# Kernel tuning notes

Measured on AMD Instinct MI355X. Metric: run time of the kernel, lower is better.

The kernel has to match this reference:

```python
import jax, jax.numpy as jnp
import numpy as np

N_HEADS = 8
TANH_CLIP = 10.0
NEG = -1e9  # finite stand-in for -inf so log_softmax/vjp stay NaN-free


def setup_inputs() -> dict:
    key = jax.random.key(0)
    ks = jax.random.split(key, 8)
    B, N, D = 256, 1000, 128
    embeddings = jax.random.normal(ks[0], (B, N, D), dtype=jnp.float32)
    W_node = jax.random.normal(ks[1], (D, 3 * D), dtype=jnp.float32) * (1.0 / np.sqrt(D))
    W_fixed = jax.random.normal(ks[2], (D, D), dtype=jnp.float32) * (1.0 / np.sqrt(D))
    W_step = jax.random.normal(ks[3], (2 * D, D), dtype=jnp.float32) * (1.0 / np.sqrt(2 * D))
    W_out = jax.random.normal(ks[4], (D, D), dtype=jnp.float32) * (1.0 / np.sqrt(D))
    first_idx = jax.random.randint(ks[5], (B,), 0, N)
    last_idx = jax.random.randint(ks[6], (B,), 0, N)
    mask = jax.random.randint(ks[7], (B, N), 0, 2).astype(jnp.bool_)
    mask = mask.at[:, 0].set(False)  # guarantee at least one feasible node
    return {"embeddings": embeddings, "W_node": W_node, "W_fixed": W_fixed,
            "W_step": W_step, "W_out": W_out, "first_idx": first_idx,
            "last_idx": last_idx, "mask": mask}


def reference(embeddings, W_node, W_fixed, W_step, W_out, first_idx, last_idx, mask):
    # One pointer-network decode step (TSP variant of AttentionModel._get_log_p),
    # including the _precompute projections.
    B, N, D = embeddings.shape
    H = N_HEADS
    dk = D // H

    # _precompute: fixed context + glimpse K/V + logit key
    graph_embed = embeddings.mean(axis=1)                       # [B, D]
    fixed_ctx = graph_embed @ W_fixed                           # [B, D]
    kvl = embeddings @ W_node                                   # [B, N, 3D]
    K, V, logit_K = jnp.split(kvl, 3, axis=-1)                  # each [B, N, D]

    # step context: cat(first-node emb, last-node emb) -> project to D
    b = jnp.arange(B)
    step_ctx = jnp.concatenate([embeddings[b, first_idx], embeddings[b, last_idx]], axis=-1)  # [B, 2D]
    q = fixed_ctx + step_ctx @ W_step                           # [B, D]

    # masked multi-head glimpse attention (q_len = 1)
    qh = q.reshape(B, H, dk)                                    # [B, H, dk]
    Kh = K.reshape(B, N, H, dk)
    Vh = V.reshape(B, N, H, dk)
    compat = jnp.einsum('bhd,bnhd->bhn', qh, Kh) / np.sqrt(dk)  # [B, H, N]
    compat = jnp.where(mask[:, None, :], NEG, compat)           # mask_inner
    attn = jax.nn.softmax(compat, axis=-1)
    heads = jnp.einsum('bhn,bnhd->bhd', attn, Vh)               # [B, H, dk]
    glimpse = heads.reshape(B, D) @ W_out                       # [B, D]

    # single-head logit attention with tanh clipping
    logits = jnp.einsum('bd,bnd->bn', glimpse, logit_K) / np.sqrt(D)  # [B, N]
    logits = jnp.tanh(logits) * TANH_CLIP
    logits = jnp.where(mask, NEG, logits)                       # mask_logits
    return jax.nn.log_softmax(logits, axis=-1)                  # [B, N]
```

## Files before the change

### kernel.cpp

```cpp
#include <hip/hip_runtime.h>


#define NEG (-1e9f)

__global__ __launch_bounds__(512, 4) void k1_mean(
    const float* __restrict__ E, float* __restrict__ muP)
{
    const int bid = blockIdx.x;
    const int b = bid & 255, half = bid >> 8;
    const int blk = b * 2 + half;
    const int t = threadIdx.x;
    const int r0g = half * 500;
    __shared__ float4 sc[512];
    const float4* E4 = (const float4*)(E + (size_t)b * 128000);
    const int cm = t & 31, sm = t >> 5;
    float4 acc = make_float4(0.f, 0.f, 0.f, 0.f);
    for (int r = sm; r < 500; r += 16) {
        const float4 v = E4[(r0g + r) * 32 + cm];
        acc.x += v.x; acc.y += v.y; acc.z += v.z; acc.w += v.w;
    }
    sc[t] = acc;
    __syncthreads();
    if (t < 32) {
        float4 a = sc[t];
        #pragma unroll
        for (int s = 1; s < 16; ++s) {
            const float4 v = sc[s * 32 + t];
            a.x += v.x; a.y += v.y; a.z += v.z; a.w += v.w;
        }
        ((float4*)(muP + (size_t)blk * 128))[t] = a;
    }
}

__global__ __launch_bounds__(512, 2) void k2_attn(
    const float* __restrict__ E, const float* __restrict__ Wn,
    const float* __restrict__ Wf, const float* __restrict__ Ws,
    const int* __restrict__ fi, const int* __restrict__ li,
    const int* __restrict__ maskI, const unsigned char* __restrict__ maskB,
    const float* __restrict__ muP, float* __restrict__ Uw,
    float* __restrict__ lw)
{
    const int bid = blockIdx.x;
    const int b = bid & 255, half = bid >> 8;
    const int blk = b * 2 + half;
    const int i0 = b * 2, i1 = i0 + 1;
    const int t = threadIdx.x;
    const int r0g = half * 500;

    __shared__ float4 Et4[2048];
    __shared__ float4 qk4[256];
    __shared__ float4 pt4[128];
    __shared__ float4 mu4[32], e14[32], e24[32];
    __shared__ float q[128];
    __shared__ float qred[4][128];
    __shared__ float ct[64 * 9];
    __shared__ float redh[72];
    __shared__ int flagS;

    float* const mu  = (float*)mu4;
    float* const e1  = (float*)e14;
    float* const e2  = (float*)e24;
    float* const pt  = (float*)pt4;
    float* const qkf = (float*)qk4;
    float* const Etf = (float*)Et4;

    const float4* E4 = (const float4*)(E + (size_t)b * 128000);

    if (t == 0) flagS = 0;
    const uint4 dv = ((const uint4*)maskI)[t];
    const unsigned det = (dv.x | dv.y | dv.z | dv.w) & 0xFFFFFF00u;

    if (t < 128) {
        mu[t] = (muP[(size_t)i0 * 128 + t] + muP[(size_t)i1 * 128 + t])
                * (1.0f / 1000.0f);
    } else if (t < 160) {
        e14[t - 128] = E4[fi[b] * 32 + (t - 128)];
    } else if (t < 192) {
        e24[t - 160] = E4[li[b] * 32 + (t - 160)];
    }
    __syncthreads();
    if (det) atomicOr(&flagS, 1);

    {
        const int part = t >> 7, d = t & 127;
        float acc = 0.f;
        const int k0 = part * 96;
        for (int k = k0; k < k0 + 96; ++k) {
            const float s = (k < 128) ? mu[k] : (k < 256 ? e1[k - 128] : e2[k - 256]);
            const float w = (k < 128) ? Wf[k * 128 + d] : Ws[(k - 128) * 128 + d];
            acc += s * w;
        }
        qred[part][d] = acc;
    }
    __syncthreads();
    if (t < 128) q[t] = qred[0][t] + qred[1][t] + qred[2][t] + qred[3][t];
    __syncthreads();
    {
        const int j = t & 127, cg = t >> 7;
        const float qj = q[j];
        for (int c0 = 0; c0 < 128; c0 += 4) {
            const int c = c0 + cg;
            float v = Wn[c * 384 + j] * qj;
            v += __shfl_down(v, 8, 16);
            v += __shfl_down(v, 4, 16);
            v += __shfl_down(v, 2, 16);
            v += __shfl_down(v, 1, 16);
            if ((j & 15) == 0) {
                const int h = j >> 4, s = c >> 2;
                qkf[h * 128 + (s ^ (s >> 2)) * 4 + (c & 3)] = v * 0.25f;
            }
        }
    }
    __syncthreads();
    const bool useB = (flagS != 0);

    float eacc[8];
    #pragma unroll
    for (int h = 0; h < 8; ++h) eacc[h] = 0.f;
    float lacc = 0.f;
    const int rr = t >> 3, qq = t & 7;
    const int esl = t >> 7, ec = t & 127;

    for (int tile = 0; tile < 8; ++tile) {
        const int lr = tile * 64 + rr;
        const bool valid = (lr < 500);
        {
            float4 v[4];
            if (valid) {
                #pragma unroll
                for (int i = 0; i < 4; ++i) v[i] = E4[(r0g + lr) * 32 + qq * 4 + i];
            } else {
                #pragma unroll
                for (int i = 0; i < 4; ++i) v[i] = make_float4(0.f, 0.f, 0.f, 0.f);
            }
            float pch[8];
            #pragma unroll
            for (int h = 0; h < 8; ++h) pch[h] = 0.f;
            #pragma unroll
            for (int i = 0; i < 4; ++i) {
                const int grp = qq * 4 + i;
                Et4[rr * 32 + grp] = v[i];
                const int sg = grp ^ (grp >> 2);
                #pragma unroll
                for (int h = 0; h < 8; ++h) {
                    const float4 w = qk4[h * 32 + sg];
                    pch[h] += v[i].x * w.x + v[i].y * w.y + v[i].z * w.z + v[i].w * w.w;
                }
            }
            #pragma unroll
            for (int m = 1; m <= 4; m <<= 1) {
                #pragma unroll
                for (int h = 0; h < 8; ++h) pch[h] += __shfl_xor(pch[h], m, 8);
            }
            bool msk = !valid;
            if (valid) msk = useB ? (maskB[b * 1000 + r0g + lr] != 0)
                                  : (maskI[b * 1000 + r0g + lr] != 0);
            ct[rr * 9 + qq] = msk ? NEG : pch[qq];
        }
        __syncthreads();
        pt[(t >> 3) * 8 + (t & 7)] = __expf(ct[(t >> 3) * 9 + (t & 7)]);
        __syncthreads();
        {
            #pragma unroll
            for (int j = 0; j < 16; ++j) {
                const int r = esl * 16 + j;
                const float ev = Etf[r * 128 + ec];
                const float4 p0 = pt4[r * 2];
                const float4 p1 = pt4[r * 2 + 1];
                eacc[0] += p0.x * ev; eacc[1] += p0.y * ev;
                eacc[2] += p0.z * ev; eacc[3] += p0.w * ev;
                eacc[4] += p1.x * ev; eacc[5] += p1.y * ev;
                eacc[6] += p1.z * ev; eacc[7] += p1.w * ev;
            }
            if (t < 64) {
                const int h = t & 7, part = t >> 3;
                #pragma unroll
                for (int r = 0; r < 8; ++r) lacc += pt[(part * 8 + r) * 8 + h];
            }
        }
        __syncthreads();
    }

    #pragma unroll
    for (int h = 0; h < 8; ++h) Etf[esl * 1024 + h * 128 + ec] = eacc[h];
    if (t < 64) redh[(t >> 3) * 9 + (t & 7)] = lacc;
    __syncthreads();
    #pragma unroll
    for (int e = 0; e < 2; ++e) {
        const int idx = t + e * 512;
        Uw[(size_t)blk * 1024 + idx] =
            Etf[idx] + Etf[1024 + idx] + Etf[2048 + idx] + Etf[3072 + idx];
    }
    if (t < 8) {
        float s = 0.f;
        #pragma unroll
        for (int p = 0; p < 8; ++p) s += redh[p * 9 + t];
        lw[blk * 8 + t] = s;
    }
}

__global__ __launch_bounds__(1024) void k3_glimpse(
    const float* __restrict__ Wn, const float* __restrict__ Wo,
    const float* __restrict__ Uw, const float* __restrict__ lw,
    float* __restrict__ gpw)
{
    const int b = blockIdx.x;
    const int t = threadIdx.x;
    const int i0 = b * 2, i1 = i0 + 1;
    __shared__ float EbarF[1024];
    __shared__ float linv[8];
    __shared__ float heads[128], gl[128];
    __shared__ float qred[8][128];
    if (t < 8) linv[t] = 1.0f / (lw[i0 * 8 + t] + lw[i1 * 8 + t]);
    __syncthreads();
    EbarF[t] = (Uw[(size_t)i0 * 1024 + t] + Uw[(size_t)i1 * 1024 + t]) * linv[t >> 7];
    __syncthreads();
    {
        const int part = t >> 7, d = t & 127, h = d >> 4;
        float acc = 0.f;
        const int c0 = part * 16;
        for (int c = c0; c < c0 + 16; ++c) acc += EbarF[h * 128 + c] * Wn[c * 384 + 128 + d];
        qred[part][d] = acc;
    }
    __syncthreads();
    if (t < 128) {
        float a = 0.f;
        #pragma unroll
        for (int p = 0; p < 8; ++p) a += qred[p][t];
        heads[t] = a;
    }
    __syncthreads();
    {
        const int part = t >> 7, d = t & 127;
        float acc = 0.f;
        const int j0 = part * 16;
        for (int j = j0; j < j0 + 16; ++j) acc += heads[j] * Wo[j * 128 + d];
        qred[part][d] = acc;
    }
    __syncthreads();
    if (t < 128) {
        float a = 0.f;
        #pragma unroll
        for (int p = 0; p < 8; ++p) a += qred[p][t];
        gl[t] = a;
    }
    __syncthreads();
    {
        const int part = t >> 7, c = t & 127;
        float acc = 0.f;
        const int d0 = part * 16;
        for (int d = d0; d < d0 + 16; ++d) acc += Wn[c * 384 + 256 + d] * gl[d];
        qred[part][c] = acc;
    }
    __syncthreads();
    if (t < 128) {
        float a = 0.f;
        #pragma unroll
        for (int p = 0; p < 8; ++p) a += qred[p][t];
        gpw[(size_t)b * 128 + t] = a * 0.08838834764831845f;
    }
}

__global__ __launch_bounds__(512, 2) void k4_logits(
    const float* __restrict__ E,
    const int* __restrict__ maskI, const unsigned char* __restrict__ maskB,
    const float* __restrict__ gpw, float* __restrict__ out,
    float* __restrict__ sw)
{
    const int bid = blockIdx.x;
    const int b = bid & 255, half = bid >> 8;
    const int blk = b * 2 + half;
    const int t = threadIdx.x;
    const int r0g = half * 500;
    __shared__ float4 gp4[32];
    __shared__ float ct[128 * 5];
    __shared__ float red[8];
    __shared__ int flagS;
    const float4* E4 = (const float4*)(E + (size_t)b * 128000);
    if (t == 0) flagS = 0;
    const uint4 dv = ((const uint4*)maskI)[t];
    const unsigned det = (dv.x | dv.y | dv.z | dv.w) & 0xFFFFFF00u;
    if (t < 32) gp4[t] = ((const float4*)(gpw + (size_t)b * 128))[t];
    __syncthreads();
    if (det) atomicOr(&flagS, 1);

    float sacc = 0.f;
    const int row = t >> 2, sub = t & 3;
    for (int tile = 0; tile < 4; ++tile) {
        const int lr = tile * 128 + row;
        float acc = 0.f;
        if (lr < 500) {
            const int g = r0g + lr;
            #pragma unroll
            for (int i = 0; i < 8; ++i) {
                const float4 v = E4[g * 32 + sub * 8 + i];
                const float4 w = gp4[sub * 8 + i];
                acc += v.x * w.x + v.y * w.y + v.z * w.z + v.w * w.w;
            }
        }
        ct[row * 5 + sub] = acc;
        __syncthreads();
        if (t < 128) {
            const int lr2 = tile * 128 + t;
            if (lr2 < 500) {
                const float s = ct[t * 5] + ct[t * 5 + 1] + ct[t * 5 + 2] + ct[t * 5 + 3];
                float zz = 10.0f * tanhf(s);
                const int g2 = r0g + lr2;
                const bool m = (flagS != 0) ? (maskB[b * 1000 + g2] != 0)
                                            : (maskI[b * 1000 + g2] != 0);
                if (m) zz = NEG;
                out[(size_t)b * 1000 + g2] = zz;
                sacc += __expf(zz - 10.0f);
            }
        }
        __syncthreads();
    }
    float sv = sacc;
    #pragma unroll
    for (int off = 32; off > 0; off >>= 1) sv += __shfl_down(sv, off, 64);
    if ((t & 63) == 0) red[t >> 6] = sv;
    __syncthreads();
    if (t == 0) {
        float s = 0.f;
        #pragma unroll
        for (int i = 0; i < 8; ++i) s += red[i];
        sw[blk] = s;
    }
}

__global__ __launch_bounds__(512, 4) void k5_norm(
    const float* __restrict__ sw, float* __restrict__ out)
{
    const int bid = blockIdx.x;
    const int b = bid & 255, half = bid >> 8;
    const int t = threadIdx.x;
    const int r0g = half * 500;
    const float s = sw[b * 2] + sw[b * 2 + 1];
    const float lse = 10.0f + __logf(s);
    if (t < 500) out[(size_t)b * 1000 + r0g + t] -= lse;
}

extern "C" void kernel_launch(void* const* d_in, const int* in_sizes, int n_in,
                              void* d_out, int out_size, void* d_ws, size_t ws_size,
                              hipStream_t stream) {
    const float* E  = (const float*)d_in[0];
    const float* Wn = (const float*)d_in[1];
    const float* Wf = (const float*)d_in[2];
    const float* Ws = (const float*)d_in[3];
    const float* Wo = (const float*)d_in[4];
    const int*   fi = (const int*)d_in[5];
    const int*   li = (const int*)d_in[6];
    const int*   maskI = (const int*)d_in[7];
    const unsigned char* maskB = (const unsigned char*)d_in[7];
    float* out = (float*)d_out;
    float* ws  = (float*)d_ws;

    float* muP = ws;
    float* Uw  = ws + 512 * 128;
    float* lw  = Uw + (size_t)512 * 1024;
    float* gpw = lw + 512 * 8;
    float* sw  = gpw + 256 * 128;

    k1_mean   <<<dim3(512), dim3(512),  0, stream>>>(E, muP);
    k2_attn   <<<dim3(512), dim3(512),  0, stream>>>(E, Wn, Wf, Ws, fi, li,
                                                     maskI, maskB, muP, Uw, lw);
    k3_glimpse<<<dim3(256), dim3(1024), 0, stream>>>(Wn, Wo, Uw, lw, gpw);
    k4_logits <<<dim3(512), dim3(512),  0, stream>>>(E, maskI, maskB, gpw, out, sw);
    k5_norm   <<<dim3(512), dim3(512),  0, stream>>>(sw, out);
}
```

Before: 348.1 us.

## Prefetch next E tile in registers and drop shared staging for scores and logits

In the attention-accumulation kernel, the first tile of embeddings and its mask are loaded before the q projection, and each following tile is prefetched into registers while the current tile is processed. The exp of the scores is now computed directly from registers, which removes one shared buffer and one barrier per tile. In the logits kernel, the per-row dot-product reduction moves from shared memory plus two barriers per tile to warp shuffles, and the loop is fully unrolled. This hides global load latency and cuts synchronisation, at the cost of more register pressure from the prefetch buffers.

New measurement: 335.6 us. -3.6%, faster.

```diff
diff --git a/kernel.cpp b/kernel.cpp
--- a/kernel.cpp
+++ b/kernel.cpp
@@ -53,7 +53,6 @@
     __shared__ float4 mu4[32], e14[32], e24[32];
     __shared__ float q[128];
     __shared__ float qred[4][128];
-    __shared__ float ct[64 * 9];
     __shared__ float redh[72];
     __shared__ int flagS;
 
@@ -65,6 +64,15 @@
     float* const Etf = (float*)Et4;
 
     const float4* E4 = (const float4*)(E + (size_t)b * 128000);
+
+    const int rr = t >> 3, qq = t & 7;
+    const int esl = t >> 7, ec = t & 127;
+
+    float4 v[4];
+    #pragma unroll
+    for (int i = 0; i < 4; ++i) v[i] = E4[(r0g + rr) * 32 + qq * 4 + i];
+    int miC = maskI[b * 1000 + r0g + rr];
+    unsigned char mbC = maskB[b * 1000 + r0g + rr];
 
     if (t == 0) flagS = 0;
     const uint4 dv = ((const uint4*)maskI)[t];
@@ -100,14 +108,14 @@
         const float qj = q[j];
         for (int c0 = 0; c0 < 128; c0 += 4) {
             const int c = c0 + cg;
-            float v = Wn[c * 384 + j] * qj;
-            v += __shfl_down(v, 8, 16);
-            v += __shfl_down(v, 4, 16);
-            v += __shfl_down(v, 2, 16);
-            v += __shfl_down(v, 1, 16);
+            float vv = Wn[c * 384 + j] * qj;
+            vv += __shfl_down(vv, 8, 16);
+            vv += __shfl_down(vv, 4, 16);
+            vv += __shfl_down(vv, 2, 16);
+            vv += __shfl_down(vv, 1, 16);
             if ((j & 15) == 0) {
                 const int h = j >> 4, s = c >> 2;
-                qkf[h * 128 + (s ^ (s >> 2)) * 4 + (c & 3)] = v * 0.25f;
+                qkf[h * 128 + (s ^ (s >> 2)) * 4 + (c & 3)] = vv * 0.25f;
             }
         }
     }
@@ -118,67 +126,67 @@
     #pragma unroll
     for (int h = 0; h < 8; ++h) eacc[h] = 0.f;
     float lacc = 0.f;
-    const int rr = t >> 3, qq = t & 7;
-    const int esl = t >> 7, ec = t & 127;
 
     for (int tile = 0; tile < 8; ++tile) {
         const int lr = tile * 64 + rr;
         const bool valid = (lr < 500);
-        {
-            float4 v[4];
-            if (valid) {
+        float pch[8];
+        #pragma unroll
+        for (int h = 0; h < 8; ++h) pch[h] = 0.f;
+        #pragma unroll
+        for (int i = 0; i < 4; ++i) {
+            const int grp = qq * 4 + i;
+            Et4[rr * 32 + grp] = v[i];
+            const int sg = grp ^ (grp >> 2);
+            #pragma unroll
+            for (int h = 0; h < 8; ++h) {
+                const float4 w = qk4[h * 32 + sg];
+                pch[h] += v[i].x * w.x + v[i].y * w.y + v[i].z * w.z + v[i].w * w.w;
+            }
+        }
+        #pragma unroll
+        for (int m = 1; m <= 4; m <<= 1) {
+            #pragma unroll
+            for (int h = 0; h < 8; ++h) pch[h] += __shfl_xor(pch[h], m, 8);
+        }
+        const bool msk = !valid || (useB ? (mbC != 0) : (miC != 0));
+        pt[rr * 8 + qq] = msk ? 0.f : __expf(pch[qq]);
+
+        float4 vn[4];
+        int miN = 1; unsigned char mbN = 1;
+        #pragma unroll
+        for (int i = 0; i < 4; ++i) vn[i] = make_float4(0.f, 0.f, 0.f, 0.f);
+        if (tile < 7) {
+            const int lr2 = lr + 64;
+            if (lr2 < 500) {
                 #pragma unroll
-                for (int i = 0; i < 4; ++i) v[i] = E4[(r0g + lr) * 32 + qq * 4 + i];
-            } else {
-                #pragma unroll
-                for (int i = 0; i < 4; ++i) v[i] = make_float4(0.f, 0.f, 0.f, 0.f);
+                for (int i = 0; i < 4; ++i)
+                    vn[i] = E4[(r0g + lr2) * 32 + qq * 4 + i];
+                miN = maskI[b * 1000 + r0g + lr2];
+                mbN = maskB[b * 1000 + r0g + lr2];
             }
-            float pch[8];
+        }
+        __syncthreads();
+        #pragma unroll
+        for (int j = 0; j < 16; ++j) {
+            const int r = esl * 16 + j;
+            const float ev = Etf[r * 128 + ec];
+            const float4 p0 = pt4[r * 2];
+            const float4 p1 = pt4[r * 2 + 1];
+            eacc[0] += p0.x * ev; eacc[1] += p0.y * ev;
+            eacc[2] += p0.z * ev; eacc[3] += p0.w * ev;
+            eacc[4] += p1.x * ev; eacc[5] += p1.y * ev;
+            eacc[6] += p1.z * ev; eacc[7] += p1.w * ev;
+        }
+        if (t < 64) {
+            const int h = t & 7, part = t >> 3;
             #pragma unroll
-            for (int h = 0; h < 8; ++h) pch[h] = 0.f;
-            #pragma unroll
-            for (int i = 0; i < 4; ++i) {
-                const int grp = qq * 4 + i;
-                Et4[rr * 32 + grp] = v[i];
-                const int sg = grp ^ (grp >> 2);
-                #pragma unroll
-                for (int h = 0; h < 8; ++h) {
-                    const float4 w = qk4[h * 32 + sg];
-                    pch[h] += v[i].x * w.x + v[i].y * w.y + v[i].z * w.z + v[i].w * w.w;
-                }
-            }
-            #pragma unroll
-            for (int m = 1; m <= 4; m <<= 1) {
-                #pragma unroll
-                for (int h = 0; h < 8; ++h) pch[h] += __shfl_xor(pch[h], m, 8);
-            }
-            bool msk = !valid;
-            if (valid) msk = useB ? (maskB[b * 1000 + r0g + lr] != 0)
-                                  : (maskI[b * 1000 + r0g + lr] != 0);
-            ct[rr * 9 + qq] = msk ? NEG : pch[qq];
+            for (int r = 0; r < 8; ++r) lacc += pt[(part * 8 + r) * 8 + h];
         }
         __syncthreads();
-        pt[(t >> 3) * 8 + (t & 7)] = __expf(ct[(t >> 3) * 9 + (t & 7)]);
-        __syncthreads();
-        {
-            #pragma unroll
-            for (int j = 0; j < 16; ++j) {
-                const int r = esl * 16 + j;
-                const float ev = Etf[r * 128 + ec];
-                const float4 p0 = pt4[r * 2];
-                const float4 p1 = pt4[r * 2 + 1];
-                eacc[0] += p0.x * ev; eacc[1] += p0.y * ev;
-                eacc[2] += p0.z * ev; eacc[3] += p0.w * ev;
-                eacc[4] += p1.x * ev; eacc[5] += p1.y * ev;
-                eacc[6] += p1.z * ev; eacc[7] += p1.w * ev;
-            }
-            if (t < 64) {
-                const int h = t & 7, part = t >> 3;
-                #pragma unroll
-                for (int r = 0; r < 8; ++r) lacc += pt[(part * 8 + r) * 8 + h];
-            }
-        }
-        __syncthreads();
+        #pragma unroll
+        for (int i = 0; i < 4; ++i) v[i] = vn[i];
+        miC = miN; mbC = mbN;
     }
 
     #pragma unroll
@@ -273,8 +281,7 @@
     const int t = threadIdx.x;
     const int r0g = half * 500;
     __shared__ float4 gp4[32];
-    __shared__ float ct[128 * 5];
-    __shared__ float red[8];
+    __shared__ float redw[8];
     __shared__ int flagS;
     const float4* E4 = (const float4*)(E + (size_t)b * 128000);
     if (t == 0) flagS = 0;
@@ -283,47 +290,44 @@
     if (t < 32) gp4[t] = ((const float4*)(gpw + (size_t)b * 128))[t];
     __syncthreads();
     if (det) atomicOr(&flagS, 1);
+    __syncthreads();
+    const bool useB = (flagS != 0);
 
     float sacc = 0.f;
     const int row = t >> 2, sub = t & 3;
+    #pragma unroll
     for (int tile = 0; tile < 4; ++tile) {
         const int lr = tile * 128 + row;
+        const int g = r0g + lr;
         float acc = 0.f;
         if (lr < 500) {
-            const int g = r0g + lr;
             #pragma unroll
             for (int i = 0; i < 8; ++i) {
-                const float4 v = E4[g * 32 + sub * 8 + i];
-                const float4 w = gp4[sub * 8 + i];
-                acc += v.x * w.x + v.y * w.y + v.z * w.z + v.w * w.w;
+                const float4 vv = E4[g * 32 + sub * 8 + i];
+                const float4 ww = gp4[sub * 8 + i];
+                acc += vv.x * ww.x + vv.y * ww.y + vv.z * ww.z + vv.w * ww.w;
             }
         }
-        ct[row * 5 + sub] = acc;
-        __syncthreads();
-        if (t < 128) {
-            const int lr2 = tile * 128 + t;
-            if (lr2 < 500) {
-                const float s = ct[t * 5] + ct[t * 5 + 1] + ct[t * 5 + 2] + ct[t * 5 + 3];
-                float zz = 10.0f * tanhf(s);
-                const int g2 = r0g + lr2;
-                const bool m = (flagS != 0) ? (maskB[b * 1000 + g2] != 0)
-                                            : (maskI[b * 1000 + g2] != 0);
-                if (m) zz = NEG;
-                out[(size_t)b * 1000 + g2] = zz;
-                sacc += __expf(zz - 10.0f);
-            }
-        }
-        __syncthreads();
+        acc += __shfl_xor(acc, 1, 4);
+        acc += __shfl_xor(acc, 2, 4);
+        if (sub == 0 && lr < 500) {
+            float zz = 10.0f * tanhf(acc);
+            const bool m = useB ? (maskB[b * 1000 + g] != 0)
+                                : (maskI[b * 1000 + g] != 0);
+            if (m) zz = NEG;
+            out[(size_t)b * 1000 + g] = zz;
+            sacc += __expf(zz - 10.0f);
+        }
     }
     float sv = sacc;
     #pragma unroll
     for (int off = 32; off > 0; off >>= 1) sv += __shfl_down(sv, off, 64);
-    if ((t & 63) == 0) red[t >> 6] = sv;
+    if ((t & 63) == 0) redw[t >> 6] = sv;
     __syncthreads();
     if (t == 0) {
         float s = 0.f;
         #pragma unroll
-        for (int i = 0; i < 8; ++i) s += red[i];
+        for (int i = 0; i < 8; ++i) s += redw[i];
         sw[blk] = s;
     }
 }
```
